# Performance work log

Measured on AMD Instinct MI355X. Metric: run time of the kernel, lower is better.

The kernel has to match this reference:

```python
import jax, jax.numpy as jnp
import numpy as np

N_NODES = 200000
N_EDGES = 4000000  # doubled (w2b + b2w), matches edge_weight param size
N_W2B = 2000000


def gcn_conv(x, W, b, src, dst, ew, n):
    # PyG GCNConv with add_self_loops=True, symmetric normalization.
    loop = jnp.arange(n)
    src_sl = jnp.concatenate([src, loop])
    dst_sl = jnp.concatenate([dst, loop])
    w_sl = jnp.concatenate([ew, jnp.ones((n,), ew.dtype)])  # self-loop weight 1
    deg = jax.ops.segment_sum(w_sl, dst_sl, num_segments=n)
    dinv = jnp.where(deg > 0, jax.lax.rsqrt(deg), 0.0)
    norm = dinv[src_sl] * w_sl * dinv[dst_sl]          # [E+N]
    xw = x @ W                                          # [N, out]
    msg = xw[src_sl] * norm[:, None]                    # [E+N, out]
    out = jax.ops.segment_sum(msg, dst_sl, num_segments=n)
    return out + b


def setup_inputs() -> dict:
    key = jax.random.key(0)
    ks = jax.random.split(key, 16)
    h1, h2, h3, h4, out = 8, 16, 32, 4, 3
    inp = 7

    def lin_init(k, fan_in, fan_out):
        bound = 1.0 / np.sqrt(fan_in)
        kw, kb = jax.random.split(k)
        W = jax.random.uniform(kw, (fan_in, fan_out), jnp.float32, -bound, bound)
        b = jax.random.uniform(kb, (fan_out,), jnp.float32, -bound, bound)
        return W, b

    x = jax.random.normal(ks[0], (N_NODES, inp), jnp.float32)
    edge_index = jax.random.randint(ks[1], (2, N_EDGES), 0, N_NODES, jnp.int64)
    w2b = jax.random.randint(ks[2], (2, N_W2B), 0, N_NODES, jnp.int64)
    edge_weight = jnp.ones((N_EDGES,), jnp.float32)  # Parameter init: ones

    W1, b1 = lin_init(ks[3], inp, h1)
    W2, b2 = lin_init(ks[4], h1, h2)
    W3, b3 = lin_init(ks[5], h2, h3)
    Wl1, bl1 = lin_init(ks[6], 2 * h3, h4)
    Wl2, bl2 = lin_init(ks[7], h4, out)

    return dict(x=x, edge_index=edge_index, w2b=w2b, edge_weight=edge_weight,
                W1=W1, b1=b1, W2=W2, b2=b2, W3=W3, b3=b3,
                Wl1=Wl1, bl1=bl1, Wl2=Wl2, bl2=bl2)


def reference(x, edge_index, w2b, edge_weight,
              W1, b1, W2, b2, W3, b3, Wl1, bl1, Wl2, bl2):
    n = x.shape[0]
    src, dst = edge_index[0], edge_index[1]
    ew = jax.nn.sigmoid(edge_weight)
    h = jax.nn.relu(gcn_conv(x, W1, b1, src, dst, ew, n))
    h = jax.nn.relu(gcn_conv(h, W2, b2, src, dst, ew, n))
    h = jax.nn.relu(gcn_conv(h, W3, b3, src, dst, ew, n))
    # fused gather-concat replacing the per-edge python loop
    concat = jnp.concatenate([h[w2b[0]], h[w2b[1]]], axis=-1)  # [E_w2b, 2*h3]
    hidden = concat @ Wl1 + bl1
    edge_pred = hidden @ Wl2 + bl2
    return edge_pred
```

## Files before the change

kernel.cpp:

```cpp
#include <hip/hip_runtime.h>
#include <hip/hip_bf16.h>
#include <hip/hip_fp16.h>


#define NB1 768
#define NPB 256
#define MAXBINS 1024
#define TILE 4096
#define QS 16384.0f
#define QINV (1.0f / 16384.0f)

typedef _Float16 h2 __attribute__((ext_vector_type(2)));
typedef _Float16 h4 __attribute__((ext_vector_type(4)));
typedef _Float16 h8 __attribute__((ext_vector_type(8)));

__device__ __forceinline__ float sigmoidf_(float x) {
    return 1.0f / (1.0f + __expf(-x));
}

__global__ void p1a_hist(const int* __restrict__ dst, int* __restrict__ bh,
                         int ne, int nbins, int chunk) {
    __shared__ int h[MAXBINS];
    for (int k = threadIdx.x; k < nbins; k += 256) h[k] = 0;
    __syncthreads();
    int base = blockIdx.x * chunk;
    int end = min(base + chunk, ne);
    for (int e = base + threadIdx.x; e < end; e += 256)
        atomicAdd(&h[dst[e] >> 8], 1);
    __syncthreads();
    for (int k = threadIdx.x; k < nbins; k += 256)
        bh[(size_t)k * NB1 + blockIdx.x] = h[k];
}

__global__ void s1_scan(int* __restrict__ bh, int* __restrict__ bintot) {
    __shared__ int sums[256];
    constexpr int W = NB1 / 256;
    int* row = bh + (size_t)blockIdx.x * NB1;
    int v[W];
    int s = 0;
#pragma unroll
    for (int j = 0; j < W; ++j) { v[j] = row[threadIdx.x * W + j]; s += v[j]; }
    sums[threadIdx.x] = s;
    __syncthreads();
    for (int o = 1; o < 256; o <<= 1) {
        int t = (threadIdx.x >= o) ? sums[threadIdx.x - o] : 0;
        __syncthreads();
        sums[threadIdx.x] += t;
        __syncthreads();
    }
    int excl = sums[threadIdx.x] - s;
#pragma unroll
    for (int j = 0; j < W; ++j) { row[threadIdx.x * W + j] = excl; excl += v[j]; }
    if (threadIdx.x == 255) bintot[blockIdx.x] = sums[255];
}

__global__ void s2_scan(const int* __restrict__ bintot, int* __restrict__ binbase,
                        int nbins, int ne) {
    __shared__ int tmp[1024];
    int tid = threadIdx.x;
    int v = (tid < nbins) ? bintot[tid] : 0;
    tmp[tid] = v;
    __syncthreads();
    for (int o = 1; o < 1024; o <<= 1) {
        int t = (tid >= o) ? tmp[tid - o] : 0;
        __syncthreads();
        tmp[tid] += t;
        __syncthreads();
    }
    if (tid < nbins) binbase[tid] = tmp[tid] - v;
    if (tid == 0) binbase[nbins] = ne;
}

__global__ void p1b_scatter(const int* __restrict__ src, const int* __restrict__ dst,
                            const float* __restrict__ ew, const int* __restrict__ bh,
                            const int* __restrict__ binbase,
                            unsigned long long* __restrict__ b64,
                            int ne, int nbins, int chunk) {
    __shared__ unsigned long long stage[TILE];
    __shared__ int hist[MAXBINS];
    __shared__ int boff[MAXBINS];
    __shared__ int cur[MAXBINS];
    __shared__ int ssum[256];
    constexpr int MPT = TILE / 256;
    for (int k = threadIdx.x; k < nbins; k += 256)
        cur[k] = binbase[k] + bh[(size_t)k * NB1 + blockIdx.x];
    int base = blockIdx.x * chunk;
    int endb = min(base + chunk, ne);
    for (int t0 = base; t0 < endb; t0 += TILE) {
        int cnt = min(TILE, endb - t0);
        for (int k = threadIdx.x; k < nbins; k += 256) hist[k] = 0;
        __syncthreads();
        unsigned long long ent[MPT];
        int m = 0;
        for (int j = threadIdx.x; j < cnt; j += 256) {
            int e = t0 + j;
            int d = dst[e];
            float w = sigmoidf_(ew[e]);
            int q = (int)fminf(w * QS + 0.5f, 16383.0f);
            int b = d >> 8;
            ent[m++] = (unsigned long long)((unsigned)src[e] | ((unsigned)q << 18))
                     | ((unsigned long long)(d & 255) << 32)
                     | ((unsigned long long)b << 40);
            atomicAdd(&hist[b], 1);
        }
        __syncthreads();
        int w0 = threadIdx.x * 4;
        int lv[4];
        int ls = 0;
#pragma unroll
        for (int j = 0; j < 4; ++j) {
            int idx = w0 + j;
            lv[j] = (idx < nbins) ? hist[idx] : 0;
            ls += lv[j];
        }
        ssum[threadIdx.x] = ls;
        __syncthreads();
        for (int o = 1; o < 256; o <<= 1) {
            int t = (threadIdx.x >= o) ? ssum[threadIdx.x - o] : 0;
            __syncthreads();
            ssum[threadIdx.x] += t;
            __syncthreads();
        }
        int excl = ssum[threadIdx.x] - ls;
#pragma unroll
        for (int j = 0; j < 4; ++j) {
            int idx = w0 + j;
            if (idx < nbins) { boff[idx] = excl; excl += lv[j]; }
        }
        __syncthreads();
        for (int k = threadIdx.x; k < nbins; k += 256) hist[k] = 0;
        __syncthreads();
        for (int j = 0; j < m; ++j) {
            int b = (int)(ent[j] >> 40);
            int p = boff[b] + atomicAdd(&hist[b], 1);
            stage[p] = ent[j];
        }
        __syncthreads();
        for (int j = threadIdx.x; j < cnt; j += 256) {
            unsigned long long v = stage[j];
            int b = (int)(v >> 40);
            b64[cur[b] + (j - boff[b])] = v;
        }
        __syncthreads();
        for (int k = threadIdx.x; k < nbins; k += 256) cur[k] += hist[k];
        __syncthreads();
    }
}

__global__ void p2_build(const unsigned long long* __restrict__ b64,
                         const int* __restrict__ binbase, unsigned* __restrict__ edata,
                         int* __restrict__ C, float* __restrict__ dinv,
                         const float* __restrict__ x, const float* __restrict__ W1,
                         _Float16* __restrict__ g0, int n, int ne, int nbins) {
    __shared__ int cnt[NPB];
    __shared__ int rs[NPB];
    __shared__ int curs[NPB];
    __shared__ unsigned qsum[NPB];
    __shared__ float Ws[56];
    if (threadIdx.x < 56) Ws[threadIdx.x] = W1[threadIdx.x];
    int b = blockIdx.x;
    int E0 = binbase[b], E1 = binbase[b + 1];
    cnt[threadIdx.x] = 0;
    qsum[threadIdx.x] = 0;
    __syncthreads();
    for (int k = E0 + threadIdx.x; k < E1; k += 256)
        atomicAdd(&cnt[(int)((b64[k] >> 32) & 0xFF)], 1);
    __syncthreads();
    int v = cnt[threadIdx.x];
    rs[threadIdx.x] = v;
    __syncthreads();
    for (int o = 1; o < NPB; o <<= 1) {
        int t = (threadIdx.x >= o) ? rs[threadIdx.x - o] : 0;
        __syncthreads();
        rs[threadIdx.x] += t;
        __syncthreads();
    }
    int excl = rs[threadIdx.x] - v;
    curs[threadIdx.x] = E0 + excl;
    int node = b * NPB + threadIdx.x;
    if (node < n) C[node] = E0 + excl;
    if (b == 0 && threadIdx.x == 0) C[n] = ne;
    __syncthreads();
    for (int k = E0 + threadIdx.x; k < E1; k += 256) {
        unsigned long long e64 = b64[k];
        int dl = (int)((e64 >> 32) & 0xFF);
        int pos = atomicAdd(&curs[dl], 1);
        edata[pos] = (unsigned)(e64 & 0xFFFFFFFFu);
        atomicAdd(&qsum[dl], (unsigned)((e64 >> 18) & 0x3FFFu));
    }
    __syncthreads();
    if (node < n) {
        float dv = rsqrtf((float)qsum[threadIdx.x] * QINV + 1.0f);
        dinv[node] = dv;
        float xi[7];
#pragma unroll
        for (int k = 0; k < 7; ++k) xi[k] = x[(size_t)node * 7 + k];
        h8 r;
#pragma unroll
        for (int o = 0; o < 8; ++o) {
            float acc = 0.0f;
#pragma unroll
            for (int k = 0; k < 7; ++k) acc = fmaf(xi[k], Ws[k * 8 + o], acc);
            r[o] = (_Float16)(acc * dv);
        }
        *reinterpret_cast<h8*>(g0 + (size_t)node * 8) = r;
    }
}

__global__ void gather1_kernel(const _Float16* __restrict__ g, const float* __restrict__ dinv,
                               const int* __restrict__ C, const unsigned* __restrict__ edata,
                               const float* __restrict__ b1, _Float16* __restrict__ out, int n) {
    __shared__ float bs[8];
    if (threadIdx.x < 8) bs[threadIdx.x] = b1[threadIdx.x];
    __syncthreads();
    long long t = (long long)blockIdx.x * blockDim.x + threadIdx.x;
    int i = (int)(t >> 3);
    int l8 = (int)(t & 7);
    if (i >= n) return;
    int beg = C[i], end = C[i + 1];
    float acc[8] = {0.f, 0.f, 0.f, 0.f, 0.f, 0.f, 0.f, 0.f};
    if (l8 == 0) {
        h8 r = *reinterpret_cast<const h8*>(g + (size_t)i * 8);
#pragma unroll
        for (int j = 0; j < 8; ++j) acc[j] = (float)r[j];
    }
    int k = beg + l8;
    for (; k + 8 < end; k += 16) {
        unsigned v0 = edata[k];
        unsigned v1 = edata[k + 8];
        h8 r0 = *reinterpret_cast<const h8*>(g + (size_t)(v0 & 0x3FFFFu) * 8);
        h8 r1 = *reinterpret_cast<const h8*>(g + (size_t)(v1 & 0x3FFFFu) * 8);
        float w0 = (float)(v0 >> 18) * QINV;
        float w1 = (float)(v1 >> 18) * QINV;
#pragma unroll
        for (int j = 0; j < 8; ++j) acc[j] = fmaf((float)r0[j], w0, acc[j]);
#pragma unroll
        for (int j = 0; j < 8; ++j) acc[j] = fmaf((float)r1[j], w1, acc[j]);
    }
    if (k < end) {
        unsigned v = edata[k];
        float w = (float)(v >> 18) * QINV;
        h8 r = *reinterpret_cast<const h8*>(g + (size_t)(v & 0x3FFFFu) * 8);
#pragma unroll
        for (int j = 0; j < 8; ++j) acc[j] = fmaf((float)r[j], w, acc[j]);
    }
    bool t4 = (l8 & 4) != 0, t2 = (l8 & 2) != 0, t1 = (l8 & 1) != 0;
    float s4[4];
#pragma unroll
    for (int j = 0; j < 4; ++j) {
        float keep = t4 ? acc[4 + j] : acc[j];
        float send = t4 ? acc[j] : acc[4 + j];
        s4[j] = keep + __shfl_xor(send, 4, 64);
    }
    float s2[2];
#pragma unroll
    for (int j = 0; j < 2; ++j) {
        float keep = t2 ? s4[2 + j] : s4[j];
        float send = t2 ? s4[j] : s4[2 + j];
        s2[j] = keep + __shfl_xor(send, 2, 64);
    }
    float keep = t1 ? s2[1] : s2[0];
    float send = t1 ? s2[0] : s2[1];
    float s = keep + __shfl_xor(send, 1, 64);
    float dv = dinv[i];
    out[(size_t)i * 8 + l8] = (_Float16)(dv * fmaxf(dv * s + bs[l8], 0.0f));
}

__global__ void gather2_kernel(const _Float16* __restrict__ g, const float* __restrict__ dinv,
                               const int* __restrict__ C, const unsigned* __restrict__ edata,
                               const float* __restrict__ W2, const float* __restrict__ b2,
                               _Float16* __restrict__ out, int n) {
    __shared__ float Ws[128];
    __shared__ float bs[16];
    if (threadIdx.x < 128) Ws[threadIdx.x] = W2[threadIdx.x];
    if (threadIdx.x < 16) bs[threadIdx.x] = b2[threadIdx.x];
    __syncthreads();
    long long t = (long long)blockIdx.x * blockDim.x + threadIdx.x;
    int i = (int)(t >> 3);
    int l8 = (int)(t & 7);
    if (i >= n) return;
    int beg = C[i], end = C[i + 1];
    float acc[8] = {0.f, 0.f, 0.f, 0.f, 0.f, 0.f, 0.f, 0.f};
    if (l8 == 0) {
        h8 r = *reinterpret_cast<const h8*>(g + (size_t)i * 8);
#pragma unroll
        for (int j = 0; j < 8; ++j) acc[j] = (float)r[j];
    }
    int k = beg + l8;
    for (; k + 8 < end; k += 16) {
        unsigned v0 = edata[k];
        unsigned v1 = edata[k + 8];
        h8 r0 = *reinterpret_cast<const h8*>(g + (size_t)(v0 & 0x3FFFFu) * 8);
        h8 r1 = *reinterpret_cast<const h8*>(g + (size_t)(v1 & 0x3FFFFu) * 8);
        float w0 = (float)(v0 >> 18) * QINV;
        float w1 = (float)(v1 >> 18) * QINV;
#pragma unroll
        for (int j = 0; j < 8; ++j) acc[j] = fmaf((float)r0[j], w0, acc[j]);
#pragma unroll
        for (int j = 0; j < 8; ++j) acc[j] = fmaf((float)r1[j], w1, acc[j]);
    }
    if (k < end) {
        unsigned v = edata[k];
        float w = (float)(v >> 18) * QINV;
        h8 r = *reinterpret_cast<const h8*>(g + (size_t)(v & 0x3FFFFu) * 8);
#pragma unroll
        for (int j = 0; j < 8; ++j) acc[j] = fmaf((float)r[j], w, acc[j]);
    }
#pragma unroll
    for (int j = 0; j < 8; ++j) {
        acc[j] += __shfl_xor(acc[j], 1, 64);
        acc[j] += __shfl_xor(acc[j], 2, 64);
        acc[j] += __shfl_xor(acc[j], 4, 64);
    }
    float dv = dinv[i];
    float raw[8];
#pragma unroll
    for (int j = 0; j < 8; ++j) raw[j] = acc[j] * dv;
    int o0 = l8 * 2;
    h2 o2;
#pragma unroll
    for (int jo = 0; jo < 2; ++jo) {
        int o = o0 + jo;
        float h = bs[o];
#pragma unroll
        for (int k2 = 0; k2 < 8; ++k2) h = fmaf(raw[k2], Ws[k2 * 16 + o], h);
        o2[jo] = (_Float16)(dv * fmaxf(h, 0.0f));
    }
    *reinterpret_cast<h2*>(out + (size_t)i * 16 + o0) = o2;
}

__global__ void gather3_kernel(const _Float16* __restrict__ g, const float* __restrict__ dinv,
                               const int* __restrict__ C, const unsigned* __restrict__ edata,
                               _Float16* __restrict__ raw3, int n) {
    long long t = (long long)blockIdx.x * blockDim.x + threadIdx.x;
    int i = (int)(t >> 3);
    int l8 = (int)(t & 7);
    if (i >= n) return;
    int beg = C[i], end = C[i + 1];
    float acc[16];
#pragma unroll
    for (int j = 0; j < 16; ++j) acc[j] = 0.0f;
    if (l8 == 0) {
        h8 r0 = *reinterpret_cast<const h8*>(g + (size_t)i * 16);
        h8 r1 = *reinterpret_cast<const h8*>(g + (size_t)i * 16 + 8);
#pragma unroll
        for (int j = 0; j < 8; ++j) { acc[j] = (float)r0[j]; acc[8 + j] = (float)r1[j]; }
    }
    int k = beg + l8;
    for (; k + 8 < end; k += 16) {
        unsigned v0 = edata[k];
        unsigned v1 = edata[k + 8];
        size_t i0 = (size_t)(v0 & 0x3FFFFu) * 16;
        size_t i1 = (size_t)(v1 & 0x3FFFFu) * 16;
        h8 a0 = *reinterpret_cast<const h8*>(g + i0);
        h8 a1 = *reinterpret_cast<const h8*>(g + i0 + 8);
        h8 c0 = *reinterpret_cast<const h8*>(g + i1);
        h8 c1 = *reinterpret_cast<const h8*>(g + i1 + 8);
        float w0 = (float)(v0 >> 18) * QINV;
        float w1 = (float)(v1 >> 18) * QINV;
#pragma unroll
        for (int j = 0; j < 8; ++j) acc[j] = fmaf((float)a0[j], w0, acc[j]);
#pragma unroll
        for (int j = 0; j < 8; ++j) acc[8 + j] = fmaf((float)a1[j], w0, acc[8 + j]);
#pragma unroll
        for (int j = 0; j < 8; ++j) acc[j] = fmaf((float)c0[j], w1, acc[j]);
#pragma unroll
        for (int j = 0; j < 8; ++j) acc[8 + j] = fmaf((float)c1[j], w1, acc[8 + j]);
    }
    if (k < end) {
        unsigned v = edata[k];
        size_t i0 = (size_t)(v & 0x3FFFFu) * 16;
        h8 a0 = *reinterpret_cast<const h8*>(g + i0);
        h8 a1 = *reinterpret_cast<const h8*>(g + i0 + 8);
        float w = (float)(v >> 18) * QINV;
#pragma unroll
        for (int j = 0; j < 8; ++j) acc[j] = fmaf((float)a0[j], w, acc[j]);
#pragma unroll
        for (int j = 0; j < 8; ++j) acc[8 + j] = fmaf((float)a1[j], w, acc[8 + j]);
    }
    bool t4 = (l8 & 4) != 0, t2 = (l8 & 2) != 0, t1 = (l8 & 1) != 0;
    float s8[8];
#pragma unroll
    for (int j = 0; j < 8; ++j) {
        float keep = t4 ? acc[8 + j] : acc[j];
        float send = t4 ? acc[j] : acc[8 + j];
        s8[j] = keep + __shfl_xor(send, 4, 64);
    }
    float s4[4];
#pragma unroll
    for (int j = 0; j < 4; ++j) {
        float keep = t2 ? s8[4 + j] : s8[j];
        float send = t2 ? s8[j] : s8[4 + j];
        s4[j] = keep + __shfl_xor(send, 2, 64);
    }
    float s2[2];
#pragma unroll
    for (int j = 0; j < 2; ++j) {
        float keep = t1 ? s4[2 + j] : s4[j];
        float send = t1 ? s4[j] : s4[2 + j];
        s2[j] = keep + __shfl_xor(send, 1, 64);
    }
    float dv = dinv[i];
    h2 o2;
    o2[0] = (_Float16)(s2[0] * dv);
    o2[1] = (_Float16)(s2[1] * dv);
    *reinterpret_cast<h2*>(raw3 + (size_t)i * 16 + l8 * 2) = o2;
}

__global__ void dense3_kernel(const _Float16* __restrict__ raw3,
                              const float* __restrict__ W3, const float* __restrict__ b3,
                              const float* __restrict__ Wl1, const float* __restrict__ bl1,
                              const float* __restrict__ Wl2, const float* __restrict__ bl2,
                              _Float16* __restrict__ pqh, int n) {
    __shared__ __align__(16) float WsT[512];
    __shared__ float bs[32];
    __shared__ float wfs[192];
    __shared__ float bfs[3];
    for (int t = threadIdx.x; t < 512; t += 256) {
        int k = t >> 5, o = t & 31;
        WsT[o * 16 + k] = W3[t];
    }
    if (threadIdx.x < 32) bs[threadIdx.x] = b3[threadIdx.x];
    if (threadIdx.x < 192) {
        int f = threadIdx.x / 3, j = threadIdx.x % 3;
        float a = 0.0f;
#pragma unroll
        for (int k = 0; k < 4; ++k) a = fmaf(Wl1[f * 4 + k], Wl2[k * 3 + j], a);
        wfs[threadIdx.x] = a;
    }
    if (threadIdx.x < 3) {
        float a = bl2[threadIdx.x];
#pragma unroll
        for (int k = 0; k < 4; ++k) a = fmaf(bl1[k], Wl2[k * 3 + threadIdx.x], a);
        bfs[threadIdx.x] = a;
    }
    __syncthreads();
    int i = blockIdx.x * 256 + threadIdx.x;
    if (i >= n) return;
    h8 r0 = *reinterpret_cast<const h8*>(raw3 + (size_t)i * 16);
    h8 r1 = *reinterpret_cast<const h8*>(raw3 + (size_t)i * 16 + 8);
    float raw[16];
#pragma unroll
    for (int j = 0; j < 8; ++j) { raw[j] = (float)r0[j]; raw[8 + j] = (float)r1[j]; }
    float p0 = bfs[0], p1 = bfs[1], p2 = bfs[2];
    float q0 = 0.0f, q1 = 0.0f, q2 = 0.0f;
#pragma unroll
    for (int o = 0; o < 32; ++o) {
        const float4* w4 = reinterpret_cast<const float4*>(WsT + o * 16);
        float4 wa = w4[0], wb = w4[1], wc = w4[2], wd = w4[3];
        float h = bs[o];
        h = fmaf(raw[0], wa.x, h);  h = fmaf(raw[1], wa.y, h);
        h = fmaf(raw[2], wa.z, h);  h = fmaf(raw[3], wa.w, h);
        h = fmaf(raw[4], wb.x, h);  h = fmaf(raw[5], wb.y, h);
        h = fmaf(raw[6], wb.z, h);  h = fmaf(raw[7], wb.w, h);
        h = fmaf(raw[8], wc.x, h);  h = fmaf(raw[9], wc.y, h);
        h = fmaf(raw[10], wc.z, h); h = fmaf(raw[11], wc.w, h);
        h = fmaf(raw[12], wd.x, h); h = fmaf(raw[13], wd.y, h);
        h = fmaf(raw[14], wd.z, h); h = fmaf(raw[15], wd.w, h);
        h = fmaxf(h, 0.0f);
        p0 = fmaf(h, wfs[o * 3 + 0], p0);
        p1 = fmaf(h, wfs[o * 3 + 1], p1);
        p2 = fmaf(h, wfs[o * 3 + 2], p2);
        q0 = fmaf(h, wfs[(32 + o) * 3 + 0], q0);
        q1 = fmaf(h, wfs[(32 + o) * 3 + 1], q1);
        q2 = fmaf(h, wfs[(32 + o) * 3 + 2], q2);
    }
    h8 o8;
    o8[0] = (_Float16)p0; o8[1] = (_Float16)p1; o8[2] = (_Float16)p2; o8[3] = (_Float16)0.0f;
    o8[4] = (_Float16)q0; o8[5] = (_Float16)q1; o8[6] = (_Float16)q2; o8[7] = (_Float16)0.0f;
    *reinterpret_cast<h8*>(pqh + (size_t)i * 8) = o8;
}

__global__ void head_kernel(const int* __restrict__ w2b, const _Float16* __restrict__ pqh,
                            float* __restrict__ out, int nw) {
    int e = blockIdx.x * blockDim.x + threadIdx.x;
    if (e >= nw) return;
    int a = w2b[e];
    int b = w2b[(size_t)nw + e];
    h4 P = *reinterpret_cast<const h4*>(pqh + (size_t)a * 8);
    h4 Q = *reinterpret_cast<const h4*>(pqh + (size_t)b * 8 + 4);
    out[(size_t)e * 3 + 0] = (float)P[0] + (float)Q[0];
    out[(size_t)e * 3 + 1] = (float)P[1] + (float)Q[1];
    out[(size_t)e * 3 + 2] = (float)P[2] + (float)Q[2];
}

extern "C" void kernel_launch(void* const* d_in, const int* in_sizes, int n_in,
                              void* d_out, int out_size, void* d_ws, size_t ws_size,
                              hipStream_t stream) {
    const float* x   = (const float*)d_in[0];
    const int* eidx  = (const int*)d_in[1];
    const int* w2b   = (const int*)d_in[2];
    const float* ew  = (const float*)d_in[3];
    const float* W1  = (const float*)d_in[4];
    const float* b1  = (const float*)d_in[5];
    const float* W2  = (const float*)d_in[6];
    const float* b2  = (const float*)d_in[7];
    const float* W3  = (const float*)d_in[8];
    const float* b3  = (const float*)d_in[9];
    const float* Wl1 = (const float*)d_in[10];
    const float* bl1 = (const float*)d_in[11];
    const float* Wl2 = (const float*)d_in[12];
    const float* bl2 = (const float*)d_in[13];
    float* out = (float*)d_out;

    const int n  = in_sizes[0] / 7;
    const int ne = in_sizes[1] / 2;
    const int nw = in_sizes[2] / 2;
    const int* src = eidx;
    const int* dst = eidx + ne;

    const int nbins = (n + NPB - 1) / NPB;
    const int chunk = (ne + NB1 - 1) / NB1;

    float*     ws      = (float*)d_ws;
    float*     dinv    = ws;
    int*       C       = (int*)(ws + n);
    unsigned*  edata   = (unsigned*)(ws + 2 * (size_t)n + 16);
    int*       bh      = (int*)(edata + ne);
    int*       bintot  = bh + (size_t)nbins * NB1;
    int*       binbase = bintot + MAXBINS;
    _Float16*  g0      = (_Float16*)(binbase + MAXBINS);
    float*     bregion = (float*)(g0 + (size_t)n * 8);
    unsigned long long* b64 = (unsigned long long*)bregion;
    _Float16*  g1      = (_Float16*)bregion;
    _Float16*  g2      = (_Float16*)(bregion + 4 * (size_t)n);
    _Float16*  pqh     = (_Float16*)(bregion + 12 * (size_t)n);
    _Float16*  raw3    = (_Float16*)(bregion + 16 * (size_t)n);

    const int Bl = 256;
    auto blks = [&](long long t) { return (int)((t + Bl - 1) / Bl); };
    const int nb8 = blks((long long)n * 8);

    p1a_hist<<<NB1, Bl, 0, stream>>>(dst, bh, ne, nbins, chunk);
    s1_scan<<<nbins, Bl, 0, stream>>>(bh, bintot);
    s2_scan<<<1, 1024, 0, stream>>>(bintot, binbase, nbins, ne);
    p1b_scatter<<<NB1, Bl, 0, stream>>>(src, dst, ew, bh, binbase, b64, ne, nbins, chunk);
    p2_build<<<nbins, Bl, 0, stream>>>(b64, binbase, edata, C, dinv, x, W1, g0, n, ne, nbins);

    gather1_kernel<<<nb8, Bl, 0, stream>>>(g0, dinv, C, edata, b1, g1, n);
    gather2_kernel<<<nb8, Bl, 0, stream>>>(g1, dinv, C, edata, W2, b2, g2, n);
    gather3_kernel<<<nb8, Bl, 0, stream>>>(g2, dinv, C, edata, raw3, n);
    dense3_kernel<<<blks(n), Bl, 0, stream>>>(raw3, W3, b3, Wl1, bl1, Wl2, bl2, pqh, n);

    head_kernel<<<blks(nw), Bl, 0, stream>>>(w2b, pqh, out, nw);
}
```

Measured before the change: 346.6 us.

## Split binned edge records into 32-bit payload plus byte key, use wave-shuffle scans

The intermediate binned edge buffer changes from 64-bit packed records to a 32-bit payload array plus a separate 1-byte local-destination array. This cuts the global traffic written by the scatter and read twice by the build kernel. The scatter kernel now counts with a separate pass over dst and places entries directly through atomics on the bin offsets, removing the register staging and second histogram pass. Both kernels swap the shared-memory Hillis-Steele scans for wavefront shuffle scans with fewer barriers. The price is re-reading dst in the scatter kernel and issuing scattered byte-sized global stores.

```diff
diff --git a/kernel.cpp b/kernel.cpp
--- a/kernel.cpp
+++ b/kernel.cpp
@@ -74,123 +74,122 @@
 __global__ void p1b_scatter(const int* __restrict__ src, const int* __restrict__ dst,
                             const float* __restrict__ ew, const int* __restrict__ bh,
                             const int* __restrict__ binbase,
-                            unsigned long long* __restrict__ b64,
+                            unsigned* __restrict__ edlo, unsigned char* __restrict__ eddl,
                             int ne, int nbins, int chunk) {
-    __shared__ unsigned long long stage[TILE];
+    __shared__ unsigned slo[TILE];
+    __shared__ unsigned shi[TILE];
     __shared__ int hist[MAXBINS];
     __shared__ int boff[MAXBINS];
     __shared__ int cur[MAXBINS];
-    __shared__ int ssum[256];
-    constexpr int MPT = TILE / 256;
-    for (int k = threadIdx.x; k < nbins; k += 256)
+    __shared__ int wsum[4];
+    int tid = threadIdx.x;
+    int lane = tid & 63, wid = tid >> 6;
+    for (int k = tid; k < nbins; k += 256)
         cur[k] = binbase[k] + bh[(size_t)k * NB1 + blockIdx.x];
     int base = blockIdx.x * chunk;
     int endb = min(base + chunk, ne);
     for (int t0 = base; t0 < endb; t0 += TILE) {
         int cnt = min(TILE, endb - t0);
-        for (int k = threadIdx.x; k < nbins; k += 256) hist[k] = 0;
-        __syncthreads();
-        unsigned long long ent[MPT];
-        int m = 0;
-        for (int j = threadIdx.x; j < cnt; j += 256) {
+        for (int k = tid; k < nbins; k += 256) hist[k] = 0;
+        __syncthreads();
+        for (int j = tid; j < cnt; j += 256)
+            atomicAdd(&hist[dst[t0 + j] >> 8], 1);
+        __syncthreads();
+        int w0 = tid * 4;
+        int lv[4];
+        int ls = 0;
+#pragma unroll
+        for (int j = 0; j < 4; ++j) {
+            lv[j] = (w0 + j < nbins) ? hist[w0 + j] : 0;
+            ls += lv[j];
+        }
+        int s = ls;
+        for (int o = 1; o < 64; o <<= 1) {
+            int t = __shfl_up(s, o, 64);
+            if (lane >= o) s += t;
+        }
+        if (lane == 63) wsum[wid] = s;
+        __syncthreads();
+        int wpre = 0;
+        for (int w = 0; w < wid; ++w) wpre += wsum[w];
+        int excl = wpre + s - ls;
+#pragma unroll
+        for (int j = 0; j < 4; ++j) {
+            if (w0 + j < nbins) { boff[w0 + j] = excl; excl += lv[j]; }
+        }
+        __syncthreads();
+        for (int j = tid; j < cnt; j += 256) {
             int e = t0 + j;
             int d = dst[e];
+            int b = d >> 8;
             float w = sigmoidf_(ew[e]);
             int q = (int)fminf(w * QS + 0.5f, 16383.0f);
-            int b = d >> 8;
-            ent[m++] = (unsigned long long)((unsigned)src[e] | ((unsigned)q << 18))
-                     | ((unsigned long long)(d & 255) << 32)
-                     | ((unsigned long long)b << 40);
-            atomicAdd(&hist[b], 1);
+            unsigned lo = (unsigned)src[e] | ((unsigned)q << 18);
+            int p = atomicAdd(&boff[b], 1);
+            slo[p] = lo;
+            shi[p] = ((unsigned)b << 8) | (unsigned)(d & 255);
         }
         __syncthreads();
-        int w0 = threadIdx.x * 4;
-        int lv[4];
-        int ls = 0;
-#pragma unroll
-        for (int j = 0; j < 4; ++j) {
-            int idx = w0 + j;
-            lv[j] = (idx < nbins) ? hist[idx] : 0;
-            ls += lv[j];
+        for (int j = tid; j < cnt; j += 256) {
+            unsigned hv = shi[j];
+            int b = (int)(hv >> 8);
+            int g = cur[b] + (j - (boff[b] - hist[b]));
+            edlo[g] = slo[j];
+            eddl[g] = (unsigned char)(hv & 255u);
         }
-        ssum[threadIdx.x] = ls;
-        __syncthreads();
-        for (int o = 1; o < 256; o <<= 1) {
-            int t = (threadIdx.x >= o) ? ssum[threadIdx.x - o] : 0;
-            __syncthreads();
-            ssum[threadIdx.x] += t;
-            __syncthreads();
-        }
-        int excl = ssum[threadIdx.x] - ls;
-#pragma unroll
-        for (int j = 0; j < 4; ++j) {
-            int idx = w0 + j;
-            if (idx < nbins) { boff[idx] = excl; excl += lv[j]; }
-        }
-        __syncthreads();
-        for (int k = threadIdx.x; k < nbins; k += 256) hist[k] = 0;
-        __syncthreads();
-        for (int j = 0; j < m; ++j) {
-            int b = (int)(ent[j] >> 40);
-            int p = boff[b] + atomicAdd(&hist[b], 1);
-            stage[p] = ent[j];
-        }
-        __syncthreads();
-        for (int j = threadIdx.x; j < cnt; j += 256) {
-            unsigned long long v = stage[j];
-            int b = (int)(v >> 40);
-            b64[cur[b] + (j - boff[b])] = v;
-        }
-        __syncthreads();
-        for (int k = threadIdx.x; k < nbins; k += 256) cur[k] += hist[k];
-        __syncthreads();
-    }
-}
-
-__global__ void p2_build(const unsigned long long* __restrict__ b64,
+        __syncthreads();
+        for (int k = tid; k < nbins; k += 256) cur[k] += hist[k];
+        __syncthreads();
+    }
+}
+
+__global__ void p2_build(const unsigned* __restrict__ edlo, const unsigned char* __restrict__ eddl,
                          const int* __restrict__ binbase, unsigned* __restrict__ edata,
                          int* __restrict__ C, float* __restrict__ dinv,
                          const float* __restrict__ x, const float* __restrict__ W1,
                          _Float16* __restrict__ g0, int n, int ne, int nbins) {
     __shared__ int cnt[NPB];
-    __shared__ int rs[NPB];
     __shared__ int curs[NPB];
     __shared__ unsigned qsum[NPB];
     __shared__ float Ws[56];
+    __shared__ int wsum[4];
     if (threadIdx.x < 56) Ws[threadIdx.x] = W1[threadIdx.x];
     int b = blockIdx.x;
     int E0 = binbase[b], E1 = binbase[b + 1];
-    cnt[threadIdx.x] = 0;
-    qsum[threadIdx.x] = 0;
-    __syncthreads();
-    for (int k = E0 + threadIdx.x; k < E1; k += 256)
-        atomicAdd(&cnt[(int)((b64[k] >> 32) & 0xFF)], 1);
-    __syncthreads();
-    int v = cnt[threadIdx.x];
-    rs[threadIdx.x] = v;
-    __syncthreads();
-    for (int o = 1; o < NPB; o <<= 1) {
-        int t = (threadIdx.x >= o) ? rs[threadIdx.x - o] : 0;
-        __syncthreads();
-        rs[threadIdx.x] += t;
-        __syncthreads();
-    }
-    int excl = rs[threadIdx.x] - v;
-    curs[threadIdx.x] = E0 + excl;
-    int node = b * NPB + threadIdx.x;
+    int tid = threadIdx.x;
+    int lane = tid & 63, wid = tid >> 6;
+    cnt[tid] = 0;
+    qsum[tid] = 0;
+    __syncthreads();
+    for (int k = E0 + tid; k < E1; k += 256)
+        atomicAdd(&cnt[(int)eddl[k]], 1);
+    __syncthreads();
+    int v = cnt[tid];
+    int s = v;
+    for (int o = 1; o < 64; o <<= 1) {
+        int t = __shfl_up(s, o, 64);
+        if (lane >= o) s += t;
+    }
+    if (lane == 63) wsum[wid] = s;
+    __syncthreads();
+    int wpre = 0;
+    for (int w = 0; w < wid; ++w) wpre += wsum[w];
+    int excl = wpre + s - v;
+    curs[tid] = E0 + excl;
+    int node = b * NPB + tid;
     if (node < n) C[node] = E0 + excl;
-    if (b == 0 && threadIdx.x == 0) C[n] = ne;
-    __syncthreads();
-    for (int k = E0 + threadIdx.x; k < E1; k += 256) {
-        unsigned long long e64 = b64[k];
-        int dl = (int)((e64 >> 32) & 0xFF);
+    if (b == 0 && tid == 0) C[n] = ne;
+    __syncthreads();
+    for (int k = E0 + tid; k < E1; k += 256) {
+        unsigned lo = edlo[k];
+        int dl = (int)eddl[k];
         int pos = atomicAdd(&curs[dl], 1);
-        edata[pos] = (unsigned)(e64 & 0xFFFFFFFFu);
-        atomicAdd(&qsum[dl], (unsigned)((e64 >> 18) & 0x3FFFu));
+        edata[pos] = lo;
+        atomicAdd(&qsum[dl], lo >> 18);
     }
     __syncthreads();
     if (node < n) {
-        float dv = rsqrtf((float)qsum[threadIdx.x] * QINV + 1.0f);
+        float dv = rsqrtf((float)qsum[tid] * QINV + 1.0f);
         dinv[node] = dv;
         float xi[7];
 #pragma unroll
@@ -521,7 +520,8 @@
     int*       binbase = bintot + MAXBINS;
     _Float16*  g0      = (_Float16*)(binbase + MAXBINS);
     float*     bregion = (float*)(g0 + (size_t)n * 8);
-    unsigned long long* b64 = (unsigned long long*)bregion;
+    unsigned*  edlo    = (unsigned*)bregion;
+    unsigned char* eddl = (unsigned char*)(edlo + ne);
     _Float16*  g1      = (_Float16*)bregion;
     _Float16*  g2      = (_Float16*)(bregion + 4 * (size_t)n);
     _Float16*  pqh     = (_Float16*)(bregion + 12 * (size_t)n);
@@ -534,8 +534,8 @@
     p1a_hist<<<NB1, Bl, 0, stream>>>(dst, bh, ne, nbins, chunk);
     s1_scan<<<nbins, Bl, 0, stream>>>(bh, bintot);
     s2_scan<<<1, 1024, 0, stream>>>(bintot, binbase, nbins, ne);
-    p1b_scatter<<<NB1, Bl, 0, stream>>>(src, dst, ew, bh, binbase, b64, ne, nbins, chunk);
-    p2_build<<<nbins, Bl, 0, stream>>>(b64, binbase, edata, C, dinv, x, W1, g0, n, ne, nbins);
+    p1b_scatter<<<NB1, Bl, 0, stream>>>(src, dst, ew, bh, binbase, edlo, eddl, ne, nbins, chunk);
+    p2_build<<<nbins, Bl, 0, stream>>>(edlo, eddl, binbase, edata, C, dinv, x, W1, g0, n, ne, nbins);
 
     gather1_kernel<<<nb8, Bl, 0, stream>>>(g0, dinv, C, edata, b1, g1, n);
     gather2_kernel<<<nb8, Bl, 0, stream>>>(g1, dinv, C, edata, W2, b2, g2, n);
```

Result: slower. 365.0 us (+5.3%).
